# Performance work log

Hardware: AMD Instinct MI355X
Metric: run time of the kernel (lower is better)

The kernel has to match this reference:

```python
import jax, jax.numpy as jnp
import numpy as np

N_HEADS = 16

def _ln(x, g, b, eps=1e-5):
    m = jnp.mean(x, axis=-1, keepdims=True)
    v = jnp.mean((x - m) ** 2, axis=-1, keepdims=True)
    return (x - m) / jnp.sqrt(v + eps) * g + b

def _gelu(x):
    return jax.nn.gelu(x, approximate=False)

def _forward(x, pos_embed, time_embed, Wint, bint, g1, be1, Wq, bq, Wk, bk, Wv, bv,
             Wo, bo, Wm1, bm1, Wm2, bm2, g2, be2, W5, b5, ew, g3, be3, Wf1, bf1, Wf2, bf2):
    B, T, C = x.shape
    H = N_HEADS
    dh = C // H
    # PositionTimingLayer: concat pos/time halves, linear, residual add
    fused = jnp.concatenate([pos_embed[:T], time_embed[:T]], axis=-1)  # [T, C]
    x = x + fused @ Wint.T + bint
    # MechanismAttention on norm1(x)
    h = _ln(x, g1, be1)
    q = (h @ Wq.T + bq).reshape(B, T, H, dh)
    k = (h @ Wk.T + bk).reshape(B, T, H, dh)
    v = (h @ Wv.T + bv).reshape(B, T, H, dh)
    scores = jnp.einsum('bthd,bshd->bhts', q, k) / np.float32(np.sqrt(dh))  # [B,H,T,T]
    mech = jax.nn.sigmoid(_gelu(h @ Wm1.T + bm1) @ Wm2.T + bm2)[..., 0]  # [B,T]
    scores = scores * (1.0 + mech[:, None, None, :])  # modulate along key dim
    attn = jax.nn.softmax(scores, axis=-1)
    ctx = jnp.einsum('bhts,bshd->bthd', attn, v).reshape(B, T, C)
    x = x + (ctx @ Wo.T + bo)
    # FiveElementsTransformationLayer on norm2(x)
    h2 = _ln(x, g2, be2)
    proj = jnp.einsum('bti,eoi->bteo', h2, W5) + b5  # [B,T,5,C]
    w = jax.nn.softmax(ew)
    x = x + jnp.einsum('e,bteo->bto', w, proj)
    # FFN on norm3(x)
    h3 = _ln(x, g3, be3)
    x = x + (_gelu(h3 @ Wf1.T + bf1) @ Wf2.T + bf2)
    return x, mech, w

def setup_inputs() -> dict:
    key = jax.random.key(0)
    d, dff, L, five = 1024, 4096, 1024, 5
    ks = jax.random.split(key, 32)
    s = 0.02
    r = lambda i, shape: jax.random.normal(ks[i], shape, dtype=jnp.float32) * s
    return {
        'x': jax.random.normal(ks[0], (4, L, d), dtype=jnp.float32),
        'pos_embed': r(1, (L, d // 2)), 'time_embed': r(2, (L, d // 2)),
        'Wint': r(3, (d, d)), 'bint': jnp.zeros((d,)),
        'g1': jnp.ones((d,)), 'be1': jnp.zeros((d,)),
        'Wq': r(4, (d, d)), 'bq': jnp.zeros((d,)),
        'Wk': r(5, (d, d)), 'bk': jnp.zeros((d,)),
        'Wv': r(6, (d, d)), 'bv': jnp.zeros((d,)),
        'Wo': r(7, (d, d)), 'bo': jnp.zeros((d,)),
        'Wm1': r(8, (d // 2, d)), 'bm1': jnp.zeros((d // 2,)),
        'Wm2': r(9, (1, d // 2)), 'bm2': jnp.zeros((1,)),
        'g2': jnp.ones((d,)), 'be2': jnp.zeros((d,)),
        'W5': r(10, (five, d, d)), 'b5': jnp.zeros((five, d)),
        'ew': jnp.ones((five,)) / five,
        'g3': jnp.ones((d,)), 'be3': jnp.zeros((d,)),
        'Wf1': r(11, (dff, d)), 'bf1': jnp.zeros((dff,)),
        'Wf2': r(12, (d, dff)), 'bf2': jnp.zeros((d,)),
    }

def reference(x, pos_embed, time_embed, Wint, bint, g1, be1, Wq, bq, Wk, bk, Wv, bv,
              Wo, bo, Wm1, bm1, Wm2, bm2, g2, be2, W5, b5, ew, g3, be3, Wf1, bf1, Wf2, bf2):
    return _forward(x, pos_embed, time_embed, Wint, bint, g1, be1, Wq, bq, Wk, bk, Wv, bv,
                    Wo, bo, Wm1, bm1, Wm2, bm2, g2, be2, W5, b5, ew, g3, be3, Wf1, bf1, Wf2, bf2)
```

## Files before the change

### kernel.cpp

```cpp
#include <hip/hip_runtime.h>

typedef unsigned short u16;
typedef __bf16 bf16_t;
typedef bf16_t bf16x8 __attribute__((ext_vector_type(8)));
typedef bf16_t bf16x4 __attribute__((ext_vector_type(4)));
typedef float f32x4 __attribute__((ext_vector_type(4)));

__device__ __forceinline__ u16 f2b(float f){
  unsigned u = __builtin_bit_cast(unsigned, f);
  u += 0x7fffu + ((u >> 16) & 1u);
  return (u16)(u >> 16);
}
__device__ __forceinline__ float b2f(u16 h){
  return __builtin_bit_cast(float, ((unsigned)h) << 16);
}
__device__ __forceinline__ float gelu_exact(float x){
  return 0.5f * x * (1.f + erff(x * 0.70710678118654752440f));
}
__device__ __forceinline__ void gld16(const void* g, void* l){
  __builtin_amdgcn_global_load_lds((const __attribute__((address_space(1))) unsigned int*)g,
                                   (__attribute__((address_space(3))) unsigned int*)l, 16, 0, 0);
}

__global__ void k_conv(const float* __restrict__ s, u16* __restrict__ d, int n){
  int i = (blockIdx.x * 256 + threadIdx.x) * 4;
  if (i >= n) return;
  float4 v = *(const float4*)(s + i);
  ushort4 o; o.x = f2b(v.x); o.y = f2b(v.y); o.z = f2b(v.z); o.w = f2b(v.w);
  *(ushort4*)(d + i) = o;
}

__global__ void k_w5(const float* __restrict__ W5, const float* __restrict__ b5,
                     const float* __restrict__ ew, u16* __restrict__ Wc,
                     float* __restrict__ b5c, float* __restrict__ outW){
  int gid = blockIdx.x * 256 + threadIdx.x;
  float e0 = ew[0], e1 = ew[1], e2 = ew[2], e3 = ew[3], e4 = ew[4];
  float mx = fmaxf(fmaxf(fmaxf(e0, e1), fmaxf(e2, e3)), e4);
  float x0 = __expf(e0 - mx), x1 = __expf(e1 - mx), x2 = __expf(e2 - mx), x3 = __expf(e3 - mx), x4 = __expf(e4 - mx);
  float inv = 1.f / (x0 + x1 + x2 + x3 + x4);
  float w0 = x0 * inv, w1 = x1 * inv, w2 = x2 * inv, w3 = x3 * inv, w4 = x4 * inv;
  float v = w0 * W5[gid] + w1 * W5[gid + 1048576] + w2 * W5[gid + 2097152]
          + w3 * W5[gid + 3145728] + w4 * W5[gid + 4194304];
  Wc[gid] = f2b(v);
  if (gid < 1024)
    b5c[gid] = w0 * b5[gid] + w1 * b5[gid + 1024] + w2 * b5[gid + 2048]
             + w3 * b5[gid + 3072] + w4 * b5[gid + 4096];
  if (gid == 0){ outW[0] = w0; outW[1] = w1; outW[2] = w2; outW[3] = w3; outW[4] = w4; }
}

__global__ void k_fused(const float* __restrict__ pos, const float* __restrict__ tim,
                        u16* __restrict__ d){
  int i = blockIdx.x * 256 + threadIdx.x;
  int t = i >> 10, c = i & 1023;
  float v = (c < 512) ? pos[t * 512 + c] : tim[t * 512 + c - 512];
  d[i] = f2b(v);
}

__global__ void k_bqkv(const float* __restrict__ bq, const float* __restrict__ bk,
                       const float* __restrict__ bv, float* __restrict__ d){
  int i = blockIdx.x * 256 + threadIdx.x;
  if (i >= 3072) return;
  d[i] = (i < 1024) ? bq[i] : (i < 2048 ? bk[i - 1024] : bv[i - 2048]);
}

__global__ void k_xinit(const float* __restrict__ xin, const float* __restrict__ tmp,
                        float* __restrict__ x){
  int i = blockIdx.x * 256 + threadIdx.x;
  float4 a = ((const float4*)xin)[i];
  float4 b = ((const float4*)tmp)[i & 262143];
  float4 o; o.x = a.x + b.x; o.y = a.y + b.y; o.z = a.z + b.z; o.w = a.w + b.w;
  ((float4*)x)[i] = o;
}

__global__ __launch_bounds__(256) void k_ln(const float* __restrict__ x, const float* __restrict__ g,
                     const float* __restrict__ be, u16* __restrict__ out){
  int row = blockIdx.x, tid = threadIdx.x;
  int w = tid >> 6, lane = tid & 63;
  const float4 v = ((const float4*)(x + (size_t)row * 1024))[tid];
  float s1 = v.x + v.y + v.z + v.w;
  float s2 = v.x * v.x + v.y * v.y + v.z * v.z + v.w * v.w;
  for (int m = 1; m < 64; m <<= 1){ s1 += __shfl_xor(s1, m, 64); s2 += __shfl_xor(s2, m, 64); }
  __shared__ float a1[4], a2[4];
  if (!lane){ a1[w] = s1; a2[w] = s2; }
  __syncthreads();
  s1 = a1[0] + a1[1] + a1[2] + a1[3];
  s2 = a2[0] + a2[1] + a2[2] + a2[3];
  float mean = s1 * (1.f / 1024.f);
  float var  = s2 * (1.f / 1024.f) - mean * mean;
  float rstd = rsqrtf(var + 1e-5f);
  float4 gv = ((const float4*)g)[tid], bv = ((const float4*)be)[tid];
  ushort4 o;
  o.x = f2b((v.x - mean) * rstd * gv.x + bv.x);
  o.y = f2b((v.y - mean) * rstd * gv.y + bv.y);
  o.z = f2b((v.z - mean) * rstd * gv.z + bv.z);
  o.w = f2b((v.w - mean) * rstd * gv.w + bv.w);
  ((ushort4*)(out + (size_t)row * 1024))[tid] = o;
}

__global__ __launch_bounds__(256) void k_mech(const u16* __restrict__ m1, const float* __restrict__ Wm2,
                      const float* __restrict__ bm2, float* __restrict__ outMech,
                      float* __restrict__ mechf){
  int tid = threadIdx.x, w = tid >> 6, lane = tid & 63;
  int r = blockIdx.x * 4 + w;
  uint4 mv = *(const uint4*)(m1 + (size_t)r * 512 + lane * 8);
  const u16* ms = (const u16*)&mv;
  float4 w0 = ((const float4*)Wm2)[lane * 2];
  float4 w1 = ((const float4*)Wm2)[lane * 2 + 1];
  float dot = b2f(ms[0]) * w0.x + b2f(ms[1]) * w0.y + b2f(ms[2]) * w0.z + b2f(ms[3]) * w0.w
            + b2f(ms[4]) * w1.x + b2f(ms[5]) * w1.y + b2f(ms[6]) * w1.z + b2f(ms[7]) * w1.w;
  for (int m = 1; m < 64; m <<= 1) dot += __shfl_xor(dot, m, 64);
  if (lane == 0){
    float z = dot + bm2[0];
    float sig = 1.f / (1.f + __expf(-z));
    outMech[r] = sig;
    mechf[r] = (1.f + sig) * 0.125f;
  }
}

__global__ __launch_bounds__(256) void k_vt(const u16* __restrict__ qkv, u16* __restrict__ vT){
  __shared__ u16 lt[64 * 64];
  const int tid = threadIdx.x;
  const int b = blockIdx.z, h = blockIdx.y, t0 = blockIdx.x * 64;
  const size_t base = (size_t)b * 1024;
#pragma unroll
  for (int i = 0; i < 2; ++i){
    int c = i * 256 + tid;
    int r = c >> 3, ch = c & 7;
    uint4 v = *(const uint4*)(qkv + (base + t0 + r) * 3072 + 2048 + h * 64 + ch * 8);
    *(uint4*)((char*)lt + r * 128 + ((ch ^ (r & 7)) << 4)) = v;
  }
  __syncthreads();
  int d = tid >> 2, tt = (tid & 3) * 16;
  u16 o[16];
#pragma unroll
  for (int j = 0; j < 16; ++j){
    int t = tt + j;
    o[j] = *(const u16*)((char*)lt + t * 128 + (((d >> 3) ^ (t & 7)) << 4) + (d & 7) * 2);
  }
  u16* dst = vT + ((size_t)(b * 16 + h) * 64 + d) * 1024 + t0 + tt;
  *(uint4*)dst = *(uint4*)&o[0];
  *(uint4*)(dst + 8) = *(uint4*)&o[8];
}

template<bool GELU_, bool RES, bool OUTF_EN, bool OUTB_EN, bool PARTIAL>
__global__ __launch_bounds__(256) void k_gemm(const u16* __restrict__ A, const u16* __restrict__ W,
                      const float* __restrict__ bias, const float* resid,
                      float* outF, u16* outB, u16* pOut, int M, int N, int K, int nbx){
  __shared__ u16 lA[3][128 * 32];
  __shared__ u16 lB[3][128 * 32];
  const int tid = threadIdx.x;
  const int w = tid >> 6, lane = tid & 63;
  const int lr = lane & 15, lg = lane >> 4;
  const int nwg = gridDim.x;
  const int q = nwg >> 3, r = nwg & 7;
  const int xcd = blockIdx.x & 7, loc = blockIdx.x >> 3;
  const int swz = (xcd < r ? xcd * (q + 1) : r * (q + 1) + (xcd - r) * q) + loc;
  const int m0 = (swz / nbx) * 128, n0 = (swz % nbx) * 128;
  const int wr = (w >> 1) * 64, wc = (w & 1) * 64;
  const int kb = blockIdx.z;
  const int Ks = K / gridDim.z;
  const int kbeg = kb * Ks;
  const int nsteps = Ks >> 5;

  f32x4 acc[4][4] = {};
  const char* gA = (const char*)A;
  const char* gW = (const char*)W;

  auto stage = [&](int buf, int k0){
#pragma unroll
    for (int i = 0; i < 2; ++i){
      int c = i * 256 + tid;
      gld16(gA + (((size_t)(m0 + (c >> 2)) * K + k0) * 2 + (c & 3) * 16),
            (char*)lA + buf * 8192 + i * 4096 + w * 1024);
      gld16(gW + (((size_t)(n0 + (c >> 2)) * K + k0) * 2 + (c & 3) * 16),
            (char*)lB + buf * 8192 + i * 4096 + w * 1024);
    }
  };

  stage(0, kbeg);
  if (nsteps > 1) stage(1, kbeg + 32);
  int cur = 0, nx = 1, pf = 2;
  for (int s = 0; s < nsteps; ++s){
    if (s + 2 < nsteps) stage(pf, kbeg + (s + 2) * 32);
    if (s + 2 < nsteps)      asm volatile("s_waitcnt vmcnt(8)" ::: "memory");
    else if (s + 1 < nsteps) asm volatile("s_waitcnt vmcnt(4)" ::: "memory");
    else                     asm volatile("s_waitcnt vmcnt(0)" ::: "memory");
    __builtin_amdgcn_s_barrier();
    bf16x8 af[4], wf[4];
#pragma unroll
    for (int mb = 0; mb < 4; ++mb)
      af[mb] = *reinterpret_cast<const bf16x8*>(&lA[cur][(wr + mb * 16 + lr) * 32 + lg * 8]);
#pragma unroll
    for (int nb = 0; nb < 4; ++nb)
      wf[nb] = *reinterpret_cast<const bf16x8*>(&lB[cur][(wc + nb * 16 + lr) * 32 + lg * 8]);
#pragma unroll
    for (int mb = 0; mb < 4; ++mb)
#pragma unroll
      for (int nb = 0; nb < 4; ++nb)
        acc[mb][nb] = __builtin_amdgcn_mfma_f32_16x16x32_bf16(af[mb], wf[nb], acc[mb][nb], 0, 0, 0);
    __builtin_amdgcn_s_barrier();
    int t = cur; cur = nx; nx = pf; pf = t;
  }

#pragma unroll
  for (int mb = 0; mb < 4; ++mb){
#pragma unroll
    for (int nb = 0; nb < 4; ++nb){
      int col = n0 + wc + nb * 16 + lr;
      float bv = PARTIAL ? 0.f : bias[col];
#pragma unroll
      for (int ii = 0; ii < 4; ++ii){
        int row = m0 + wr + mb * 16 + lg * 4 + ii;
        float v = acc[mb][nb][ii] + bv;
        if (GELU_) v = gelu_exact(v);
        size_t idx = (size_t)row * N + col;
        if (RES) v += resid[idx];
        if (PARTIAL) pOut[(size_t)kb * M * N + idx] = f2b(v);
        if (OUTF_EN) outF[idx] = v;
        if (OUTB_EN) outB[idx] = f2b(v);
      }
    }
  }
}

__global__ __launch_bounds__(256) void k_red(const u16* __restrict__ pw, const float* __restrict__ bias,
                     const float* __restrict__ resid, float* __restrict__ outF, int MN, int N){
  int i = (blockIdx.x * 256 + threadIdx.x) * 8;
  uint4 v0 = *(const uint4*)(pw + i);
  uint4 v1 = *(const uint4*)(pw + MN + i);
  const u16* a = (const u16*)&v0;
  const u16* b = (const u16*)&v1;
  int col = i & (N - 1);
  float4 bv0 = *(const float4*)(bias + col);
  float4 bv1 = *(const float4*)(bias + col + 4);
  float4 r0 = *(const float4*)(resid + i);
  float4 r1 = *(const float4*)(resid + i + 4);
  float4 o0, o1;
  o0.x = b2f(a[0]) + b2f(b[0]) + bv0.x + r0.x;
  o0.y = b2f(a[1]) + b2f(b[1]) + bv0.y + r0.y;
  o0.z = b2f(a[2]) + b2f(b[2]) + bv0.z + r0.z;
  o0.w = b2f(a[3]) + b2f(b[3]) + bv0.w + r0.w;
  o1.x = b2f(a[4]) + b2f(b[4]) + bv1.x + r1.x;
  o1.y = b2f(a[5]) + b2f(b[5]) + bv1.y + r1.y;
  o1.z = b2f(a[6]) + b2f(b[6]) + bv1.z + r1.z;
  o1.w = b2f(a[7]) + b2f(b[7]) + bv1.w + r1.w;
  *(float4*)(outF + i) = o0;
  *(float4*)(outF + i + 4) = o1;
}

__global__ __launch_bounds__(256) void k_attn(const u16* __restrict__ qkv, const u16* __restrict__ vT,
                      const float* __restrict__ mechf, u16* __restrict__ ctx){
  __shared__ u16 lk[64 * 64];
  __shared__ u16 lvt[64 * 64];
  __shared__ u16 lpt[4][64 * 16];
  __shared__ float lmf[64];
  const int tid = threadIdx.x, w = tid >> 6, lane = tid & 63;
  const int lr = lane & 15, lg = lane >> 4;
  const int b = blockIdx.z, h = blockIdx.y, q0 = blockIdx.x * 64;
  const size_t base = (size_t)b * 1024;
  const size_t bh = (size_t)(b * 16 + h);

  bf16x8 qf[2];
  {
    const u16* qrow = qkv + (base + q0 + w * 16 + lr) * 3072 + h * 64;
    qf[0] = *(const bf16x8*)(qrow + lg * 8);
    qf[1] = *(const bf16x8*)(qrow + 32 + lg * 8);
  }
  float m_i[4], l_i[4];
  f32x4 cacc[4] = {};
#pragma unroll
  for (int i = 0; i < 4; ++i){ m_i[i] = -1e30f; l_i[i] = 0.f; }

  char* lkb = (char*)lk;
  char* lvb = (char*)lvt;
  unsigned lpw = (unsigned)(uintptr_t)(__attribute__((address_space(3))) u16*)&lpt[w][0];
  unsigned ta = lpw + lg * 256 + lr * 8;

  for (int jt = 0; jt < 1024; jt += 64){
    __syncthreads();
#pragma unroll
    for (int i = 0; i < 2; ++i){
      int c = i * 256 + tid;
      int row = c >> 3, ch = c & 7;
      int chs = ch ^ (row & 7);
      gld16(qkv + (base + jt + row) * 3072 + 1024 + h * 64 + chs * 8,
            lkb + i * 4096 + w * 1024);
      gld16(vT + (bh * 64 + row) * 1024 + jt + chs * 8,
            lvb + i * 4096 + w * 1024);
    }
    if (tid < 64) lmf[tid] = mechf[base + jt + tid];
    __syncthreads();

    f32x4 s[4];
    __builtin_amdgcn_s_setprio(1);
#pragma unroll
    for (int kb = 0; kb < 4; ++kb){
      int row = kb * 16 + lr;
      bf16x8 kf0 = *(const bf16x8*)(lkb + row * 128 + ((lg ^ (row & 7)) << 4));
      bf16x8 kf1 = *(const bf16x8*)(lkb + row * 128 + (((4 + lg) ^ (row & 7)) << 4));
      f32x4 z = {};
      z = __builtin_amdgcn_mfma_f32_16x16x32_bf16(qf[0], kf0, z, 0, 0, 0);
      z = __builtin_amdgcn_mfma_f32_16x16x32_bf16(qf[1], kf1, z, 0, 0, 0);
      float f = lmf[row];
      s[kb] = z * f;
    }
    __builtin_amdgcn_s_setprio(0);

    float tm[4];
#pragma unroll
    for (int i = 0; i < 4; ++i)
      tm[i] = fmaxf(fmaxf(s[0][i], s[1][i]), fmaxf(s[2][i], s[3][i]));
#pragma unroll
    for (int off = 1; off < 16; off <<= 1)
#pragma unroll
      for (int i = 0; i < 4; ++i) tm[i] = fmaxf(tm[i], __shfl_xor(tm[i], off, 64));
    float sc[4];
#pragma unroll
    for (int i = 0; i < 4; ++i){
      float mn = fmaxf(m_i[i], tm[i]);
      sc[i] = __expf(m_i[i] - mn);
      m_i[i] = mn;
    }
#pragma unroll
    for (int kb = 0; kb < 4; ++kb){
      ushort4 pk;
      float p0 = __expf(s[kb][0] - m_i[0]); s[kb][0] = p0; pk.x = f2b(p0);
      float p1 = __expf(s[kb][1] - m_i[1]); s[kb][1] = p1; pk.y = f2b(p1);
      float p2 = __expf(s[kb][2] - m_i[2]); s[kb][2] = p2; pk.z = f2b(p2);
      float p3 = __expf(s[kb][3] - m_i[3]); s[kb][3] = p3; pk.w = f2b(p3);
      *(uint2*)((char*)&lpt[w][0] + (kb * 16 + lr) * 32 + lg * 8) =
          __builtin_bit_cast(uint2, pk);
    }
#pragma unroll
    for (int i = 0; i < 4; ++i){
      float r = (s[0][i] + s[1][i]) + (s[2][i] + s[3][i]);
#pragma unroll
      for (int off = 1; off < 16; off <<= 1) r += __shfl_xor(r, off, 64);
      l_i[i] = l_i[i] * sc[i] + r;
#pragma unroll
      for (int db = 0; db < 4; ++db) cacc[db][i] *= sc[i];
    }

    asm volatile("s_waitcnt lgkmcnt(0)" ::: "memory");
    bf16x4 t00, t01, t10, t11;
    asm volatile("ds_read_b64_tr_b16 %0, %1 offset:0"    : "=v"(t00) : "v"(ta));
    asm volatile("ds_read_b64_tr_b16 %0, %1 offset:128"  : "=v"(t01) : "v"(ta));
    asm volatile("ds_read_b64_tr_b16 %0, %1 offset:1024" : "=v"(t10) : "v"(ta));
    asm volatile("ds_read_b64_tr_b16 %0, %1 offset:1152" : "=v"(t11) : "v"(ta));
    asm volatile("s_waitcnt lgkmcnt(0)");
    __builtin_amdgcn_sched_barrier(0);
    bf16x8 pf0 = __builtin_shufflevector(t00, t01, 0, 1, 2, 3, 4, 5, 6, 7);
    bf16x8 pf1 = __builtin_shufflevector(t10, t11, 0, 1, 2, 3, 4, 5, 6, 7);

    __builtin_amdgcn_s_setprio(1);
#pragma unroll
    for (int db = 0; db < 4; ++db){
      int row = db * 16 + lr;
      bf16x8 vf0 = *(const bf16x8*)(lvb + row * 128 + ((lg ^ (row & 7)) << 4));
      bf16x8 vf1 = *(const bf16x8*)(lvb + row * 128 + (((4 + lg) ^ (row & 7)) << 4));
      cacc[db] = __builtin_amdgcn_mfma_f32_16x16x32_bf16(pf0, vf0, cacc[db], 0, 0, 0);
      cacc[db] = __builtin_amdgcn_mfma_f32_16x16x32_bf16(pf1, vf1, cacc[db], 0, 0, 0);
    }
    __builtin_amdgcn_s_setprio(0);
  }
  size_t orow0 = base + q0 + w * 16;
#pragma unroll
  for (int db = 0; db < 4; ++db)
#pragma unroll
    for (int i = 0; i < 4; ++i)
      ctx[(orow0 + lg * 4 + i) * 1024 + h * 64 + db * 16 + lr] = f2b(cacc[db][i] / l_i[i]);
}

extern "C" void kernel_launch(void* const* d_in, const int* in_sizes, int n_in,
                              void* d_out, int out_size, void* d_ws, size_t ws_size,
                              hipStream_t stream){
  const float* x_in = (const float*)d_in[0];
  const float* pos  = (const float*)d_in[1];
  const float* tim  = (const float*)d_in[2];
  const float* Wint = (const float*)d_in[3];
  const float* bint = (const float*)d_in[4];
  const float* g1   = (const float*)d_in[5];
  const float* be1  = (const float*)d_in[6];
  const float* Wq   = (const float*)d_in[7];
  const float* bq   = (const float*)d_in[8];
  const float* Wk   = (const float*)d_in[9];
  const float* bk   = (const float*)d_in[10];
  const float* Wv   = (const float*)d_in[11];
  const float* bv   = (const float*)d_in[12];
  const float* Wo   = (const float*)d_in[13];
  const float* bo   = (const float*)d_in[14];
  const float* Wm1  = (const float*)d_in[15];
  const float* bm1  = (const float*)d_in[16];
  const float* Wm2  = (const float*)d_in[17];
  const float* bm2  = (const float*)d_in[18];
  const float* g2   = (const float*)d_in[19];
  const float* be2  = (const float*)d_in[20];
  const float* W5   = (const float*)d_in[21];
  const float* b5   = (const float*)d_in[22];
  const float* ew   = (const float*)d_in[23];
  const float* g3   = (const float*)d_in[24];
  const float* be3  = (const float*)d_in[25];
  const float* Wf1  = (const float*)d_in[26];
  const float* bf1  = (const float*)d_in[27];
  const float* Wf2  = (const float*)d_in[28];
  const float* bf2  = (const float*)d_in[29];

  float* outX = (float*)d_out;
  float* outM = outX + 4194304;
  float* outW = outX + 4198400;

  char* p = (char*)d_ws;
  auto alloc = [&](size_t bytes) -> char* {
    char* r = p; p += (bytes + 255) & ~(size_t)255; return r;
  };
  u16* Wint_b = (u16*)alloc(1048576 * 2);
  u16* Wqkv_b = (u16*)alloc(3145728 * 2);
  u16* Wm1_b  = (u16*)alloc(524288 * 2);
  u16* Wo_b   = (u16*)alloc(1048576 * 2);
  u16* Wc_b   = (u16*)alloc(1048576 * 2);
  u16* Wf1_b  = (u16*)alloc(4194304 * 2);
  u16* Wf2_b  = (u16*)alloc(4194304 * 2);
  u16* fus_b  = (u16*)alloc(1048576 * 2);
  float* bqkv = (float*)alloc(3072 * 4);
  float* b5c  = (float*)alloc(1024 * 4);
  float* mechf= (float*)alloc(4096 * 4);
  float* tmpF = (float*)alloc(1048576 * 4);
  float* xbuf = (float*)alloc(4194304 * 4);
  u16* h_b    = (u16*)alloc(4194304 * 2);
  char* big   = alloc(36 * 1024 * 1024);
  u16* qkv_b  = (u16*)big;
  u16* m1_b   = (u16*)(big + 24 * 1024 * 1024);
  u16* ctx_b  = (u16*)(big + 28 * 1024 * 1024);
  u16* f1_b   = (u16*)big;
  u16* vT_b   = h_b;
  u16* pw_b   = (u16*)d_ws;

  dim3 blk(256);
  k_conv<<<1024, blk, 0, stream>>>(Wint, Wint_b, 1048576);
  k_conv<<<1024, blk, 0, stream>>>(Wq, Wqkv_b, 1048576);
  k_conv<<<1024, blk, 0, stream>>>(Wk, Wqkv_b + 1048576, 1048576);
  k_conv<<<1024, blk, 0, stream>>>(Wv, Wqkv_b + 2097152, 1048576);
  k_conv<<<512,  blk, 0, stream>>>(Wm1, Wm1_b, 524288);
  k_conv<<<1024, blk, 0, stream>>>(Wo, Wo_b, 1048576);
  k_conv<<<4096, blk, 0, stream>>>(Wf1, Wf1_b, 4194304);
  k_conv<<<4096, blk, 0, stream>>>(Wf2, Wf2_b, 4194304);
  k_w5<<<4096, blk, 0, stream>>>(W5, b5, ew, Wc_b, b5c, outW);
  k_fused<<<4096, blk, 0, stream>>>(pos, tim, fus_b);
  k_bqkv<<<12, blk, 0, stream>>>(bq, bk, bv, bqkv);

  k_gemm<false,false,true,false,false><<<dim3(64, 1, 1), blk, 0, stream>>>(
      fus_b, Wint_b, bint, nullptr, tmpF, nullptr, nullptr, 1024, 1024, 1024, 8);
  k_xinit<<<4096, blk, 0, stream>>>(x_in, tmpF, xbuf);

  k_ln<<<4096, blk, 0, stream>>>(xbuf, g1, be1, h_b);
  k_gemm<false,false,false,true,false><<<dim3(768, 1, 1), blk, 0, stream>>>(
      h_b, Wqkv_b, bqkv, nullptr, nullptr, qkv_b, nullptr, 4096, 3072, 1024, 24);
  k_gemm<true,false,false,true,false><<<dim3(128, 1, 1), blk, 0, stream>>>(
      h_b, Wm1_b, bm1, nullptr, nullptr, m1_b, nullptr, 4096, 512, 1024, 4);
  k_mech<<<1024, blk, 0, stream>>>(m1_b, Wm2, bm2, outM, mechf);
  k_vt<<<dim3(16, 16, 4), blk, 0, stream>>>(qkv_b, vT_b);
  k_attn<<<dim3(16, 16, 4), blk, 0, stream>>>(qkv_b, vT_b, mechf, ctx_b);
  k_gemm<false,true,true,false,false><<<dim3(256, 1, 1), blk, 0, stream>>>(
      ctx_b, Wo_b, bo, xbuf, xbuf, nullptr, nullptr, 4096, 1024, 1024, 8);

  k_ln<<<4096, blk, 0, stream>>>(xbuf, g2, be2, h_b);
  k_gemm<false,true,true,false,false><<<dim3(256, 1, 1), blk, 0, stream>>>(
      h_b, Wc_b, b5c, xbuf, xbuf, nullptr, nullptr, 4096, 1024, 1024, 8);

  k_ln<<<4096, blk, 0, stream>>>(xbuf, g3, be3, h_b);
  k_gemm<true,false,false,true,false><<<dim3(1024, 1, 1), blk, 0, stream>>>(
      h_b, Wf1_b, bf1, nullptr, nullptr, f1_b, nullptr, 4096, 4096, 1024, 32);
  k_gemm<false,false,false,false,true><<<dim3(256, 1, 2), blk, 0, stream>>>(
      f1_b, Wf2_b, nullptr, nullptr, nullptr, nullptr, pw_b, 4096, 1024, 4096, 8);
  k_red<<<2048, blk, 0, stream>>>(pw_b, bf2, xbuf, outX, 4194304, 1024);
}
```

Baseline: 575.0 us.

## Batch weight conversions, add 256-row GEMM tile, and strip-swizzle block mapping

Replaces eight separate fp32-to-bf16 weight conversion launches with one segmented kernel to cut launch overhead. The GEMM kernel gains a BM template parameter, and the FFN up-projection uses 256x128 tiles with half as many blocks, which raises arithmetic intensity per block. It also remaps block indices into column strips of 8 N-tiles so blocks resident together share W tiles in cache. The larger tile doubles accumulator registers and LDS use for A, which may lower occupancy.

```diff
diff --git a/kernel.cpp b/kernel.cpp
--- a/kernel.cpp
+++ b/kernel.cpp
@@ -22,12 +22,18 @@
                                    (__attribute__((address_space(3))) unsigned int*)l, 16, 0, 0);
 }
 
-__global__ void k_conv(const float* __restrict__ s, u16* __restrict__ d, int n){
-  int i = (blockIdx.x * 256 + threadIdx.x) * 4;
-  if (i >= n) return;
-  float4 v = *(const float4*)(s + i);
+struct ConvArgs { const float* s[8]; u16* d[8]; unsigned cum[8]; };
+
+__global__ __launch_bounds__(256) void k_convall(ConvArgs a){
+  unsigned g = blockIdx.x * 256 + threadIdx.x;
+  int seg = 0;
+#pragma unroll
+  for (int i = 0; i < 7; ++i) seg += (g >= a.cum[i]);
+  unsigned base = seg ? a.cum[seg - 1] : 0u;
+  unsigned idx = (g - base) * 4;
+  float4 v = *(const float4*)(a.s[seg] + idx);
   ushort4 o; o.x = f2b(v.x); o.y = f2b(v.y); o.z = f2b(v.z); o.w = f2b(v.w);
-  *(ushort4*)(d + i) = o;
+  *(ushort4*)(a.d[seg] + idx) = o;
 }
 
 __global__ void k_w5(const float* __restrict__ W5, const float* __restrict__ b5,
@@ -142,11 +148,14 @@
   *(uint4*)(dst + 8) = *(uint4*)&o[8];
 }
 
-template<bool GELU_, bool RES, bool OUTF_EN, bool OUTB_EN, bool PARTIAL>
+template<bool GELU_, bool RES, bool OUTF_EN, bool OUTB_EN, bool PARTIAL, int BM>
 __global__ __launch_bounds__(256) void k_gemm(const u16* __restrict__ A, const u16* __restrict__ W,
                       const float* __restrict__ bias, const float* resid,
                       float* outF, u16* outB, u16* pOut, int M, int N, int K, int nbx){
-  __shared__ u16 lA[3][128 * 32];
+  constexpr int MB = BM / 32;
+  constexpr int ACH = BM * 4;
+  constexpr int AIT = ACH / 256;
+  __shared__ u16 lA[3][BM * 32];
   __shared__ u16 lB[3][128 * 32];
   const int tid = threadIdx.x;
   const int w = tid >> 6, lane = tid & 63;
@@ -155,23 +164,32 @@
   const int q = nwg >> 3, r = nwg & 7;
   const int xcd = blockIdx.x & 7, loc = blockIdx.x >> 3;
   const int swz = (xcd < r ? xcd * (q + 1) : r * (q + 1) + (xcd - r) * q) + loc;
-  const int m0 = (swz / nbx) * 128, n0 = (swz % nbx) * 128;
-  const int wr = (w >> 1) * 64, wc = (w & 1) * 64;
+  const int nby = nwg / nbx;
+  const int SW = (nbx & 7) ? nbx : 8;
+  const int ss = nby * SW;
+  const int strip = swz / ss, rem = swz % ss;
+  const int m0 = (rem / SW) * BM;
+  const int n0 = (strip * SW + rem % SW) * 128;
+  const int wr = (w >> 1) * (BM / 2), wc = (w & 1) * 64;
   const int kb = blockIdx.z;
   const int Ks = K / gridDim.z;
   const int kbeg = kb * Ks;
   const int nsteps = Ks >> 5;
 
-  f32x4 acc[4][4] = {};
+  f32x4 acc[MB][4] = {};
   const char* gA = (const char*)A;
   const char* gW = (const char*)W;
 
   auto stage = [&](int buf, int k0){
 #pragma unroll
+    for (int i = 0; i < AIT; ++i){
+      int c = i * 256 + tid;
+      gld16(gA + (((size_t)(m0 + (c >> 2)) * K + k0) * 2 + (c & 3) * 16),
+            (char*)lA + buf * (BM * 64) + i * 4096 + w * 1024);
+    }
+#pragma unroll
     for (int i = 0; i < 2; ++i){
       int c = i * 256 + tid;
-      gld16(gA + (((size_t)(m0 + (c >> 2)) * K + k0) * 2 + (c & 3) * 16),
-            (char*)lA + buf * 8192 + i * 4096 + w * 1024);
       gld16(gW + (((size_t)(n0 + (c >> 2)) * K + k0) * 2 + (c & 3) * 16),
             (char*)lB + buf * 8192 + i * 4096 + w * 1024);
     }
@@ -182,19 +200,25 @@
   int cur = 0, nx = 1, pf = 2;
   for (int s = 0; s < nsteps; ++s){
     if (s + 2 < nsteps) stage(pf, kbeg + (s + 2) * 32);
-    if (s + 2 < nsteps)      asm volatile("s_waitcnt vmcnt(8)" ::: "memory");
-    else if (s + 1 < nsteps) asm volatile("s_waitcnt vmcnt(4)" ::: "memory");
-    else                     asm volatile("s_waitcnt vmcnt(0)" ::: "memory");
+    if (s + 2 < nsteps){
+      if (BM == 256) asm volatile("s_waitcnt vmcnt(12)" ::: "memory");
+      else           asm volatile("s_waitcnt vmcnt(8)"  ::: "memory");
+    } else if (s + 1 < nsteps){
+      if (BM == 256) asm volatile("s_waitcnt vmcnt(6)" ::: "memory");
+      else           asm volatile("s_waitcnt vmcnt(4)" ::: "memory");
+    } else {
+      asm volatile("s_waitcnt vmcnt(0)" ::: "memory");
+    }
     __builtin_amdgcn_s_barrier();
-    bf16x8 af[4], wf[4];
-#pragma unroll
-    for (int mb = 0; mb < 4; ++mb)
+    bf16x8 af[MB], wf[4];
+#pragma unroll
+    for (int mb = 0; mb < MB; ++mb)
       af[mb] = *reinterpret_cast<const bf16x8*>(&lA[cur][(wr + mb * 16 + lr) * 32 + lg * 8]);
 #pragma unroll
     for (int nb = 0; nb < 4; ++nb)
       wf[nb] = *reinterpret_cast<const bf16x8*>(&lB[cur][(wc + nb * 16 + lr) * 32 + lg * 8]);
 #pragma unroll
-    for (int mb = 0; mb < 4; ++mb)
+    for (int mb = 0; mb < MB; ++mb)
 #pragma unroll
       for (int nb = 0; nb < 4; ++nb)
         acc[mb][nb] = __builtin_amdgcn_mfma_f32_16x16x32_bf16(af[mb], wf[nb], acc[mb][nb], 0, 0, 0);
@@ -203,7 +227,7 @@
   }
 
 #pragma unroll
-  for (int mb = 0; mb < 4; ++mb){
+  for (int mb = 0; mb < MB; ++mb){
 #pragma unroll
     for (int nb = 0; nb < 4; ++nb){
       int col = n0 + wc + nb * 16 + lr;
@@ -436,41 +460,45 @@
   u16* pw_b   = (u16*)d_ws;
 
   dim3 blk(256);
-  k_conv<<<1024, blk, 0, stream>>>(Wint, Wint_b, 1048576);
-  k_conv<<<1024, blk, 0, stream>>>(Wq, Wqkv_b, 1048576);
-  k_conv<<<1024, blk, 0, stream>>>(Wk, Wqkv_b + 1048576, 1048576);
-  k_conv<<<1024, blk, 0, stream>>>(Wv, Wqkv_b + 2097152, 1048576);
-  k_conv<<<512,  blk, 0, stream>>>(Wm1, Wm1_b, 524288);
-  k_conv<<<1024, blk, 0, stream>>>(Wo, Wo_b, 1048576);
-  k_conv<<<4096, blk, 0, stream>>>(Wf1, Wf1_b, 4194304);
-  k_conv<<<4096, blk, 0, stream>>>(Wf2, Wf2_b, 4194304);
+  ConvArgs ca;
+  ca.s[0] = Wint; ca.d[0] = Wint_b;
+  ca.s[1] = Wq;   ca.d[1] = Wqkv_b;
+  ca.s[2] = Wk;   ca.d[2] = Wqkv_b + 1048576;
+  ca.s[3] = Wv;   ca.d[3] = Wqkv_b + 2097152;
+  ca.s[4] = Wm1;  ca.d[4] = Wm1_b;
+  ca.s[5] = Wo;   ca.d[5] = Wo_b;
+  ca.s[6] = Wf1;  ca.d[6] = Wf1_b;
+  ca.s[7] = Wf2;  ca.d[7] = Wf2_b;
+  ca.cum[0] = 262144;  ca.cum[1] = 524288;  ca.cum[2] = 786432;  ca.cum[3] = 1048576;
+  ca.cum[4] = 1179648; ca.cum[5] = 1441792; ca.cum[6] = 2490368; ca.cum[7] = 3538944;
+  k_convall<<<13824, blk, 0, stream>>>(ca);
   k_w5<<<4096, blk, 0, stream>>>(W5, b5, ew, Wc_b, b5c, outW);
   k_fused<<<4096, blk, 0, stream>>>(pos, tim, fus_b);
   k_bqkv<<<12, blk, 0, stream>>>(bq, bk, bv, bqkv);
 
-  k_gemm<false,false,true,false,false><<<dim3(64, 1, 1), blk, 0, stream>>>(
+  k_gemm<false,false,true,false,false,128><<<dim3(64, 1, 1), blk, 0, stream>>>(
       fus_b, Wint_b, bint, nullptr, tmpF, nullptr, nullptr, 1024, 1024, 1024, 8);
   k_xinit<<<4096, blk, 0, stream>>>(x_in, tmpF, xbuf);
 
   k_ln<<<4096, blk, 0, stream>>>(xbuf, g1, be1, h_b);
-  k_gemm<false,false,false,true,false><<<dim3(768, 1, 1), blk, 0, stream>>>(
+  k_gemm<false,false,false,true,false,128><<<dim3(768, 1, 1), blk, 0, stream>>>(
       h_b, Wqkv_b, bqkv, nullptr, nullptr, qkv_b, nullptr, 4096, 3072, 1024, 24);
-  k_gemm<true,false,false,true,false><<<dim3(128, 1, 1), blk, 0, stream>>>(
+  k_gemm<true,false,false,true,false,128><<<dim3(128, 1, 1), blk, 0, stream>>>(
       h_b, Wm1_b, bm1, nullptr, nullptr, m1_b, nullptr, 4096, 512, 1024, 4);
   k_mech<<<1024, blk, 0, stream>>>(m1_b, Wm2, bm2, outM, mechf);
   k_vt<<<dim3(16, 16, 4), blk, 0, stream>>>(qkv_b, vT_b);
   k_attn<<<dim3(16, 16, 4), blk, 0, stream>>>(qkv_b, vT_b, mechf, ctx_b);
-  k_gemm<false,true,true,false,false><<<dim3(256, 1, 1), blk, 0, stream>>>(
+  k_gemm<false,true,true,false,false,128><<<dim3(256, 1, 1), blk, 0, stream>>>(
       ctx_b, Wo_b, bo, xbuf, xbuf, nullptr, nullptr, 4096, 1024, 1024, 8);
 
   k_ln<<<4096, blk, 0, stream>>>(xbuf, g2, be2, h_b);
-  k_gemm<false,true,true,false,false><<<dim3(256, 1, 1), blk, 0, stream>>>(
+  k_gemm<false,true,true,false,false,128><<<dim3(256, 1, 1), blk, 0, stream>>>(
       h_b, Wc_b, b5c, xbuf, xbuf, nullptr, nullptr, 4096, 1024, 1024, 8);
 
   k_ln<<<4096, blk, 0, stream>>>(xbuf, g3, be3, h_b);
-  k_gemm<true,false,false,true,false><<<dim3(1024, 1, 1), blk, 0, stream>>>(
+  k_gemm<true,false,false,true,false,256><<<dim3(512, 1, 1), blk, 0, stream>>>(
       h_b, Wf1_b, bf1, nullptr, nullptr, f1_b, nullptr, 4096, 4096, 1024, 32);
-  k_gemm<false,false,false,false,true><<<dim3(256, 1, 2), blk, 0, stream>>>(
+  k_gemm<false,false,false,false,true,128><<<dim3(256, 1, 2), blk, 0, stream>>>(
       f1_b, Wf2_b, nullptr, nullptr, nullptr, nullptr, pw_b, 4096, 1024, 4096, 8);
   k_red<<<2048, blk, 0, stream>>>(pw_b, bf2, xbuf, outX, 4194304, 1024);
 }
```

Result: slower. 592.5 us (+3.0%).
